# Kernel tuning notes

Hardware: AMD Instinct MI355X
Metric: run time of the kernel (lower is better)

The kernel has to match this reference:

```python
import jax, jax.numpy as jnp
import numpy as np

EMBED_DIM = 1024
NUM_HEADS = 16
HEAD_DIM = EMBED_DIM // NUM_HEADS
BATCH = 4
SEQ = 2048


def setup_inputs() -> dict:
    key = jax.random.key(0)
    k1, k2, k3 = jax.random.split(key, 3)
    scale = 0.02
    x = jax.random.normal(k1, (BATCH, SEQ, EMBED_DIM), dtype=jnp.float32)
    Wqkv = jax.random.normal(k2, (EMBED_DIM, 3 * EMBED_DIM), dtype=jnp.float32) * scale
    bqkv = jnp.zeros((3 * EMBED_DIM,), dtype=jnp.float32)
    Wout = jax.random.normal(k3, (EMBED_DIM, EMBED_DIM), dtype=jnp.float32) * scale
    bout = jnp.zeros((EMBED_DIM,), dtype=jnp.float32)
    # causal mask: 1 where attention is allowed (lower triangle), 0 elsewhere
    mask = jnp.tril(jnp.ones((SEQ, SEQ), dtype=jnp.int32))
    return {"x": x, "mask": mask, "Wqkv": Wqkv, "bqkv": bqkv, "Wout": Wout, "bout": bout}


def reference(x, mask, Wqkv, bqkv, Wout, bout):
    B, S, E = x.shape
    H, D = NUM_HEADS, HEAD_DIM
    qkv = x @ Wqkv + bqkv                      # [B,S,3E]
    qkv = qkv.reshape(B, S, 3, H, D)
    qkv = jnp.transpose(qkv, (2, 0, 3, 1, 4))  # [3,B,H,S,D]
    Q, K, V = qkv[0], qkv[1], qkv[2]
    scores = jnp.einsum('bhqd,bhkd->bhqk', Q, K) / jnp.sqrt(jnp.float32(D))
    scores = jnp.where(mask[None, None] == 0, jnp.float32(-jnp.inf), scores)
    attn = jax.nn.softmax(scores, axis=-1)     # dropout omitted (eval mode)
    out = jnp.einsum('bhqk,bhkd->bhqd', attn, V)
    out = jnp.transpose(out, (0, 2, 1, 3)).reshape(B, S, E)
    return out @ Wout + bout
```

## Files before the change

kernel.cpp:

```cpp
#include <hip/hip_runtime.h>

#define S_LEN 2048
#define NH    16
#define HD    64
#define EMB   1024
#define NB    4
#define MROWS (NB * S_LEN)

typedef __attribute__((ext_vector_type(8))) short  short8;
typedef __attribute__((ext_vector_type(4))) float  float4_t;
typedef __attribute__((ext_vector_type(4))) int    int4_t;
union U8 { int4_t i; short8 s; };

__device__ __forceinline__ unsigned short f2bf(float f) {
    unsigned int x = __float_as_uint(f);
    unsigned int r = (x + 0x7fffu + ((x >> 16) & 1u)) >> 16;
    return (unsigned short)r;
}

typedef const __attribute__((address_space(1))) unsigned int* gas_ptr;
typedef __attribute__((address_space(3))) unsigned int*       las_ptr;
__device__ __forceinline__ void gld_lds16(const void* g, void* l) {
    __builtin_amdgcn_global_load_lds((gas_ptr)g, (las_ptr)l, 16, 0, 0);
}

#define QSCALE 0.18033688011112042f

__global__ void cvt_f32_bf16(const float* __restrict__ in,
                             unsigned short* __restrict__ out, int n2) {
    int i = blockIdx.x * blockDim.x + threadIdx.x;
    if (i < n2) {
        float2 v = ((const float2*)in)[i];
        ushort2 o; o.x = f2bf(v.x); o.y = f2bf(v.y);
        ((ushort2*)out)[i] = o;
    }
}

__global__ void transpose_f32_bf16(const float* __restrict__ in,
                                   unsigned short* __restrict__ out, int R, int C) {
    __shared__ float tile[32][33];
    int n0 = blockIdx.x * 32, r0 = blockIdx.y * 32;
    int tx = threadIdx.x, ty = threadIdx.y;
#pragma unroll
    for (int i = 0; i < 4; ++i)
        tile[ty + i * 8][tx] = in[(size_t)(r0 + ty + i * 8) * C + n0 + tx];
    __syncthreads();
#pragma unroll
    for (int i = 0; i < 4; ++i)
        out[(size_t)(n0 + ty + i * 8) * R + r0 + tx] = f2bf(tile[tx][ty + i * 8]);
}

__global__ __launch_bounds__(256) void gemm_qkv(
    const unsigned short* __restrict__ X,
    const unsigned short* __restrict__ WT,
    const float* __restrict__ bias,
    unsigned short* __restrict__ Qb,
    unsigned short* __restrict__ Kb,
    unsigned short* __restrict__ VTb)
{
    __shared__ alignas(16) unsigned short As[128 * 32];
    __shared__ alignas(16) unsigned short Bs[128 * 32];
    const int K = 1024;
    int t = threadIdx.x;
    int wave = t >> 6, lane = t & 63, quad = lane >> 4, l = lane & 15;
    int bm = blockIdx.x * 128, bn = blockIdx.y * 128;
    int wm = (wave >> 1) * 64, wn = (wave & 1) * 64;

    float4_t z = {0.f, 0.f, 0.f, 0.f};
    float4_t acc[4][4];
#pragma unroll
    for (int i = 0; i < 4; ++i)
#pragma unroll
        for (int j = 0; j < 4; ++j) acc[i][j] = z;

    for (int kt = 0; kt < K / 32; ++kt) {
        int k0 = kt * 32;
        if (kt) __syncthreads();
#pragma unroll
        for (int it = 0; it < 2; ++it) {
            int c = t + 256 * it;
            int row = c >> 2, col = (c & 3) * 8;
            gld_lds16(&X [(size_t)(bm + row) * K + k0 + col], &As[c * 8]);
            gld_lds16(&WT[(size_t)(bn + row) * K + k0 + col], &Bs[c * 8]);
        }
        __syncthreads();
        short8 af[4], bfr[4];
#pragma unroll
        for (int i = 0; i < 4; ++i)
            af[i] = *(const short8*)&As[(wm + i * 16 + l) * 32 + quad * 8];
#pragma unroll
        for (int j = 0; j < 4; ++j)
            bfr[j] = *(const short8*)&Bs[(wn + j * 16 + l) * 32 + quad * 8];
#pragma unroll
        for (int i = 0; i < 4; ++i)
#pragma unroll
            for (int j = 0; j < 4; ++j)
                acc[i][j] = __builtin_amdgcn_mfma_f32_16x16x32_bf16(
                    af[i], bfr[j], acc[i][j], 0, 0, 0);
    }
#pragma unroll
    for (int j = 0; j < 4; ++j) {
        int gc = bn + wn + j * 16 + l;
        float bv = bias[gc];
        int which = gc >> 10, rem = gc & 1023;
        int h = rem >> 6, d = rem & 63;
        if (which == 2) {
            int bb = bm >> 11;
            size_t rowbase = ((size_t)(bb * NH + h) * HD + d) * S_LEN;
#pragma unroll
            for (int i = 0; i < 4; ++i) {
                unsigned int u0 = __float_as_uint(acc[i][j][0] + bv) + 0x8000u;
                unsigned int u1 = __float_as_uint(acc[i][j][1] + bv) + 0x8000u;
                unsigned int u2 = __float_as_uint(acc[i][j][2] + bv) + 0x8000u;
                unsigned int u3 = __float_as_uint(acc[i][j][3] + bv) + 0x8000u;
                uint2 vv;
                vv.x = __builtin_amdgcn_perm(u1, u0, 0x07060302u);
                vv.y = __builtin_amdgcn_perm(u3, u2, 0x07060302u);
                int s0 = (bm + wm + i * 16 + quad * 4) & 2047;
                int k6 = s0 & 63;
                int s0p = (s0 & ~63) | (((k6 >> 2) & 3) << 4) | (((k6 >> 4) & 3) << 2);
                *(uint2*)&VTb[rowbase + s0p] = vv;
            }
        } else {
#pragma unroll
            for (int i = 0; i < 4; ++i)
#pragma unroll
                for (int r = 0; r < 4; ++r) {
                    int gr = bm + wm + i * 16 + quad * 4 + r;
                    int b = gr >> 11, s = gr & 2047;
                    float ov = acc[i][j][r] + bv;
                    size_t bh2 = (size_t)(b * NH + h);
                    if (which == 0) Qb[(bh2 * S_LEN + s) * HD + d] = f2bf(ov * QSCALE);
                    else            Kb[(bh2 * S_LEN + s) * HD + d] = f2bf(ov);
                }
        }
    }
}

__global__ __launch_bounds__(256, 2) void flash_attn(
    const unsigned short* __restrict__ Qb,
    const unsigned short* __restrict__ Kb,
    const unsigned short* __restrict__ VTb,
    unsigned short* __restrict__ AO)
{
    __shared__ alignas(16) unsigned short smem[16384];

    int t = threadIdx.x, wave = t >> 6, lane = t & 63, quad = lane >> 4, cl = lane & 15;
    int blk = blockIdx.x;
    int bh = (blk & 7) + 8 * ((blk >> 3) & 7);
    int g = blk >> 6;
    int b = bh >> 4, h = bh & 15;
    int ci = (wave & 2) ? (62 - 2 * g + (wave & 1)) : (2 * g + (wave & 1));
    int qb = 32 * ci;
    int nkt = (ci >> 1) + 1;
    int nkt_max = 32 - g;

    const unsigned short* Qbase = Qb  + (size_t)bh * S_LEN * HD;
    const unsigned short* Kbase = Kb  + (size_t)bh * S_LEN * HD;
    const unsigned short* Vbase = VTb + (size_t)bh * HD * S_LEN;

    float4_t z = {0.f, 0.f, 0.f, 0.f};
    short8 onesf;
#pragma unroll
    for (int i = 0; i < 8; ++i) onesf[i] = (short)0x3F80;

    short8 bQ[2][2];
#pragma unroll
    for (int qt = 0; qt < 2; ++qt)
#pragma unroll
        for (int hh = 0; hh < 2; ++hh)
            bQ[qt][hh] = *(const short8*)&Qbase[(size_t)(qb + qt * 16 + cl) * HD + hh * 32 + quad * 8];

    float4_t acc[2][4], accs[2];
#pragma unroll
    for (int qt = 0; qt < 2; ++qt) {
        accs[qt] = z;
#pragma unroll
        for (int nb = 0; nb < 4; ++nb) acc[qt][nb] = z;
    }

    int koff0[4], koff1[4];
#pragma unroll
    for (int t4 = 0; t4 < 4; ++t4) {
        int row = t4 * 16 + cl, sw = row & 7;
        koff0[t4] = (row << 7) | ((quad ^ sw) << 4);
        koff1[t4] = (row << 7) | (((quad + 4) ^ sw) << 4);
    }
    int voffB[2][4];
#pragma unroll
    for (int p = 0; p < 2; ++p)
#pragma unroll
        for (int nb = 0; nb < 4; ++nb) {
            int row = nb * 16 + cl;
            voffB[p][nb] = 8192 + ((row << 7) | (((quad * 2 + p) ^ (row & 7)) << 4));
        }

    auto stage = [&](int u) {
        int key0 = u << 6;
        unsigned short* Kd = smem + (u & 1) * 8192;
        unsigned short* Vd = Kd + 4096;
#pragma unroll
        for (int i = 0; i < 2; ++i) {
            int s = t + 256 * i;
            int row = s >> 3, c16 = (s & 7) ^ (row & 7);
            gld_lds16(&Kbase[(size_t)(key0 + row) * HD + c16 * 8], &Kd[s * 8]);
            gld_lds16(&Vbase[(size_t)row * S_LEN + key0 + c16 * 8], &Vd[s * 8]);
        }
    };

    stage(0);
    for (int u = 0; u < nkt_max; ++u) {
        __syncthreads();
        if (u + 1 < nkt_max) stage(u + 1);
        if (u < nkt) {
            const char* Kc = (const char*)(smem + (u & 1) * 8192);
            int key0 = u << 6;
            short8 aK0[4], aK1[4];
#pragma unroll
            for (int t4 = 0; t4 < 4; ++t4) {
                aK0[t4] = *(const short8*)(Kc + koff0[t4]);
                aK1[t4] = *(const short8*)(Kc + koff1[t4]);
            }
            U8 bv[2][4];
#pragma unroll
            for (int p = 0; p < 2; ++p)
#pragma unroll
                for (int nb = 0; nb < 4; ++nb)
                    bv[p][nb].i = *(const int4_t*)(Kc + voffB[p][nb]);

            bool diag = (u == nkt - 1);
#pragma unroll
            for (int qt = 0; qt < 2; ++qt) {
                unsigned int pk[4][2];
#pragma unroll
                for (int t4 = 0; t4 < 4; ++t4) {
                    float4_t st = __builtin_amdgcn_mfma_f32_16x16x32_bf16(
                        aK1[t4], bQ[qt][1],
                        __builtin_amdgcn_mfma_f32_16x16x32_bf16(aK0[t4], bQ[qt][0], z, 0, 0, 0),
                        0, 0, 0);
                    unsigned int u4[4];
#pragma unroll
                    for (int r = 0; r < 4; ++r) {
                        float e = __builtin_amdgcn_exp2f(st[r]);
                        if (diag) {
                            int key = key0 + t4 * 16 + quad * 4 + r;
                            e = (key <= qb + qt * 16 + cl) ? e : 0.f;
                        }
                        u4[r] = __float_as_uint(e) + 0x8000u;
                    }
                    pk[t4][0] = __builtin_amdgcn_perm(u4[1], u4[0], 0x07060302u);
                    pk[t4][1] = __builtin_amdgcn_perm(u4[3], u4[2], 0x07060302u);
                }
#pragma unroll
                for (int p = 0; p < 2; ++p) {
                    U8 a; a.i = (int4_t){(int)pk[2 * p][0], (int)pk[2 * p][1],
                                         (int)pk[2 * p + 1][0], (int)pk[2 * p + 1][1]};
                    accs[qt] = __builtin_amdgcn_mfma_f32_16x16x32_bf16(
                        a.s, onesf, accs[qt], 0, 0, 0);
#pragma unroll
                    for (int nb = 0; nb < 4; ++nb)
                        acc[qt][nb] = __builtin_amdgcn_mfma_f32_16x16x32_bf16(
                            a.s, bv[p][nb].s, acc[qt][nb], 0, 0, 0);
                }
            }
        }
    }

    __syncthreads();
    unsigned short* stgw = smem + wave * 1088;

#pragma unroll
    for (int qt = 0; qt < 2; ++qt) {
        float fr[4];
#pragma unroll
        for (int r = 0; r < 4; ++r) fr[r] = 1.f / accs[qt][r];
#pragma unroll
        for (int nb = 0; nb < 4; ++nb)
#pragma unroll
            for (int r = 0; r < 4; ++r) {
                unsigned int uu = __float_as_uint(acc[qt][nb][r] * fr[r]) + 0x8000u;
                stgw[(quad * 4 + r) * 68 + nb * 16 + cl] = (unsigned short)(uu >> 16);
            }
#pragma unroll
        for (int pass = 0; pass < 4; ++pass) {
            int idx = pass * 64 + lane;
            int row = idx >> 4, part = idx & 15;
            ushort4 v = *(const ushort4*)&stgw[row * 68 + part * 4];
            *(ushort4*)&AO[((size_t)b * S_LEN + qb + qt * 16 + row) * EMB + h * HD + part * 4] = v;
        }
    }
}

__global__ __launch_bounds__(256) void gemm_out(
    const unsigned short* __restrict__ A,
    const unsigned short* __restrict__ WT,
    const float* __restrict__ bias,
    float* __restrict__ out)
{
    __shared__ alignas(16) unsigned short As[128 * 32];
    __shared__ alignas(16) unsigned short Bs[128 * 32];
    const int K = 1024;
    int t = threadIdx.x;
    int wave = t >> 6, lane = t & 63, quad = lane >> 4, l = lane & 15;
    int bm = blockIdx.x * 128, bn = blockIdx.y * 128;
    int wm = (wave >> 1) * 64, wn = (wave & 1) * 64;

    float4_t z = {0.f, 0.f, 0.f, 0.f};
    float4_t acc[4][4];
#pragma unroll
    for (int i = 0; i < 4; ++i)
#pragma unroll
        for (int j = 0; j < 4; ++j) acc[i][j] = z;

    for (int kt = 0; kt < K / 32; ++kt) {
        int k0 = kt * 32;
        if (kt) __syncthreads();
#pragma unroll
        for (int it = 0; it < 2; ++it) {
            int c = t + 256 * it;
            int row = c >> 2, col = (c & 3) * 8;
            gld_lds16(&A [(size_t)(bm + row) * K + k0 + col], &As[c * 8]);
            gld_lds16(&WT[(size_t)(bn + row) * K + k0 + col], &Bs[c * 8]);
        }
        __syncthreads();
        short8 af[4], bfr[4];
#pragma unroll
        for (int i = 0; i < 4; ++i)
            af[i] = *(const short8*)&As[(wm + i * 16 + l) * 32 + quad * 8];
#pragma unroll
        for (int j = 0; j < 4; ++j)
            bfr[j] = *(const short8*)&Bs[(wn + j * 16 + l) * 32 + quad * 8];
#pragma unroll
        for (int i = 0; i < 4; ++i)
#pragma unroll
            for (int j = 0; j < 4; ++j)
                acc[i][j] = __builtin_amdgcn_mfma_f32_16x16x32_bf16(
                    af[i], bfr[j], acc[i][j], 0, 0, 0);
    }
#pragma unroll
    for (int j = 0; j < 4; ++j) {
        int gc = bn + wn + j * 16 + l;
        float bv = bias[gc];
#pragma unroll
        for (int i = 0; i < 4; ++i) {
#pragma unroll
            for (int r = 0; r < 4; ++r) {
                int gr = bm + wm + i * 16 + quad * 4 + r;
                out[(size_t)gr * EMB + gc] = acc[i][j][r] + bv;
            }
        }
    }
}

extern "C" void kernel_launch(void* const* d_in, const int* in_sizes, int n_in,
                              void* d_out, int out_size, void* d_ws, size_t ws_size,
                              hipStream_t stream) {
    const float* x    = (const float*)d_in[0];
    const float* Wqkv = (const float*)d_in[2];
    const float* bqkv = (const float*)d_in[3];
    const float* Wout = (const float*)d_in[4];
    const float* bout = (const float*)d_in[5];
    float* out = (float*)d_out;

    char* ws = (char*)d_ws;
    const size_t SZ = (size_t)NB * NH * S_LEN * HD * 2;
    unsigned short* Qb    = (unsigned short*)(ws);
    unsigned short* Kb    = (unsigned short*)(ws + SZ);
    unsigned short* VTb   = (unsigned short*)(ws + 2 * SZ);
    unsigned short* Xb    = (unsigned short*)(ws + 3 * SZ);
    unsigned short* AO    = (unsigned short*)(ws + 3 * SZ);
    unsigned short* WqkvT = (unsigned short*)(ws + 4 * SZ);
    unsigned short* WoutT = (unsigned short*)(ws + 4 * SZ + (size_t)3 * EMB * EMB * 2);

    int n2 = MROWS * EMB / 2;
    cvt_f32_bf16<<<dim3((n2 + 255) / 256), 256, 0, stream>>>(x, Xb, n2);
    dim3 tb(32, 8);
    transpose_f32_bf16<<<dim3(3 * EMB / 32, EMB / 32), tb, 0, stream>>>(Wqkv, WqkvT, EMB, 3 * EMB);
    transpose_f32_bf16<<<dim3(EMB / 32, EMB / 32), tb, 0, stream>>>(Wout, WoutT, EMB, EMB);
    gemm_qkv<<<dim3(MROWS / 128, 3 * EMB / 128), 256, 0, stream>>>(Xb, WqkvT, bqkv, Qb, Kb, VTb);
    flash_attn<<<dim3(1024), 256, 0, stream>>>(Qb, Kb, VTb, AO);
    gemm_out<<<dim3(MROWS / 128, EMB / 128), 256, 0, stream>>>(AO, WoutT, bout, out);
}
```

Baseline: 270.0 us.

## Triple-buffer K/V tiles with explicit vmcnt waits and templated diagonal path

Moves the flash-attention K/V staging from double to triple buffering in LDS. Tiles are prefetched two steps ahead, and the loop waits with explicit s_waitcnt vmcnt plus a raw s_barrier instead of __syncthreads, so global-to-LDS loads overlap more compute. The diagonal masking is split into a compile-time template so non-diagonal tiles skip the mask code, and the P conversion to bf16 now uses the v_cvt_pk_bf16_f32 instruction. LDS use grows from 32KB to 48KB per block, which may limit occupancy, and the hand-written vmcnt counts must match the number of outstanding loads.

```diff
diff --git a/kernel.cpp b/kernel.cpp
--- a/kernel.cpp
+++ b/kernel.cpp
@@ -18,11 +18,19 @@
     return (unsigned short)r;
 }
 
+__device__ __forceinline__ unsigned int cvtpk_bf16(float lo, float hi) {
+    unsigned int r;
+    asm("v_cvt_pk_bf16_f32 %0, %1, %2" : "=v"(r) : "v"(lo), "v"(hi));
+    return r;
+}
+
 typedef const __attribute__((address_space(1))) unsigned int* gas_ptr;
 typedef __attribute__((address_space(3))) unsigned int*       las_ptr;
 __device__ __forceinline__ void gld_lds16(const void* g, void* l) {
     __builtin_amdgcn_global_load_lds((gas_ptr)g, (las_ptr)l, 16, 0, 0);
 }
+
+template<bool B> struct BoolC { static constexpr bool v = B; };
 
 #define QSCALE 0.18033688011112042f
 
@@ -143,7 +151,7 @@
     const unsigned short* __restrict__ VTb,
     unsigned short* __restrict__ AO)
 {
-    __shared__ alignas(16) unsigned short smem[16384];
+    __shared__ alignas(16) unsigned short smem[24576];
 
     int t = threadIdx.x, wave = t >> 6, lane = t & 63, quad = lane >> 4, cl = lane & 15;
     int blk = blockIdx.x;
@@ -195,9 +203,9 @@
             voffB[p][nb] = 8192 + ((row << 7) | (((quad * 2 + p) ^ (row & 7)) << 4));
         }
 
-    auto stage = [&](int u) {
-        int key0 = u << 6;
-        unsigned short* Kd = smem + (u & 1) * 8192;
+    auto stage = [&](int kt, int slot) {
+        int key0 = kt << 6;
+        unsigned short* Kd = smem + slot * 8192;
         unsigned short* Vd = Kd + 4096;
 #pragma unroll
         for (int i = 0; i < 2; ++i) {
@@ -208,62 +216,75 @@
         }
     };
 
-    stage(0);
+    auto compute = [&](auto DIAGC, int slot, int key0) {
+        constexpr bool DIAG = decltype(DIAGC)::v;
+        const char* Kc = (const char*)(smem + slot * 8192);
+        short8 aK0[4], aK1[4];
+#pragma unroll
+        for (int t4 = 0; t4 < 4; ++t4) {
+            aK0[t4] = *(const short8*)(Kc + koff0[t4]);
+            aK1[t4] = *(const short8*)(Kc + koff1[t4]);
+        }
+        U8 bv[2][4];
+#pragma unroll
+        for (int p = 0; p < 2; ++p)
+#pragma unroll
+            for (int nb = 0; nb < 4; ++nb)
+                bv[p][nb].i = *(const int4_t*)(Kc + voffB[p][nb]);
+
+#pragma unroll
+        for (int qt = 0; qt < 2; ++qt) {
+            unsigned int pk[4][2];
+#pragma unroll
+            for (int t4 = 0; t4 < 4; ++t4) {
+                float4_t st = __builtin_amdgcn_mfma_f32_16x16x32_bf16(
+                    aK1[t4], bQ[qt][1],
+                    __builtin_amdgcn_mfma_f32_16x16x32_bf16(aK0[t4], bQ[qt][0], z, 0, 0, 0),
+                    0, 0, 0);
+                float e[4];
+#pragma unroll
+                for (int r = 0; r < 4; ++r) {
+                    e[r] = __builtin_amdgcn_exp2f(st[r]);
+                    if (DIAG) {
+                        int key = key0 + t4 * 16 + quad * 4 + r;
+                        e[r] = (key <= qb + qt * 16 + cl) ? e[r] : 0.f;
+                    }
+                }
+                pk[t4][0] = cvtpk_bf16(e[0], e[1]);
+                pk[t4][1] = cvtpk_bf16(e[2], e[3]);
+            }
+#pragma unroll
+            for (int p = 0; p < 2; ++p) {
+                U8 a; a.i = (int4_t){(int)pk[2 * p][0], (int)pk[2 * p][1],
+                                     (int)pk[2 * p + 1][0], (int)pk[2 * p + 1][1]};
+                accs[qt] = __builtin_amdgcn_mfma_f32_16x16x32_bf16(
+                    a.s, onesf, accs[qt], 0, 0, 0);
+#pragma unroll
+                for (int nb = 0; nb < 4; ++nb)
+                    acc[qt][nb] = __builtin_amdgcn_mfma_f32_16x16x32_bf16(
+                        a.s, bv[p][nb].s, acc[qt][nb], 0, 0, 0);
+            }
+        }
+    };
+
+    stage(0, 0);
+    if (nkt_max > 1) stage(1, 1);
+    int cb = 0, sb = 2;
     for (int u = 0; u < nkt_max; ++u) {
-        __syncthreads();
-        if (u + 1 < nkt_max) stage(u + 1);
+        if (u + 1 < nkt_max) {
+            asm volatile("s_waitcnt vmcnt(4)" ::: "memory");
+        } else {
+            asm volatile("s_waitcnt vmcnt(0)" ::: "memory");
+        }
+        __builtin_amdgcn_s_barrier();
+        __builtin_amdgcn_sched_barrier(0);
+        if (u + 2 < nkt_max) stage(u + 2, sb);
         if (u < nkt) {
-            const char* Kc = (const char*)(smem + (u & 1) * 8192);
-            int key0 = u << 6;
-            short8 aK0[4], aK1[4];
-#pragma unroll
-            for (int t4 = 0; t4 < 4; ++t4) {
-                aK0[t4] = *(const short8*)(Kc + koff0[t4]);
-                aK1[t4] = *(const short8*)(Kc + koff1[t4]);
-            }
-            U8 bv[2][4];
-#pragma unroll
-            for (int p = 0; p < 2; ++p)
-#pragma unroll
-                for (int nb = 0; nb < 4; ++nb)
-                    bv[p][nb].i = *(const int4_t*)(Kc + voffB[p][nb]);
-
-            bool diag = (u == nkt - 1);
-#pragma unroll
-            for (int qt = 0; qt < 2; ++qt) {
-                unsigned int pk[4][2];
-#pragma unroll
-                for (int t4 = 0; t4 < 4; ++t4) {
-                    float4_t st = __builtin_amdgcn_mfma_f32_16x16x32_bf16(
-                        aK1[t4], bQ[qt][1],
-                        __builtin_amdgcn_mfma_f32_16x16x32_bf16(aK0[t4], bQ[qt][0], z, 0, 0, 0),
-                        0, 0, 0);
-                    unsigned int u4[4];
-#pragma unroll
-                    for (int r = 0; r < 4; ++r) {
-                        float e = __builtin_amdgcn_exp2f(st[r]);
-                        if (diag) {
-                            int key = key0 + t4 * 16 + quad * 4 + r;
-                            e = (key <= qb + qt * 16 + cl) ? e : 0.f;
-                        }
-                        u4[r] = __float_as_uint(e) + 0x8000u;
-                    }
-                    pk[t4][0] = __builtin_amdgcn_perm(u4[1], u4[0], 0x07060302u);
-                    pk[t4][1] = __builtin_amdgcn_perm(u4[3], u4[2], 0x07060302u);
-                }
-#pragma unroll
-                for (int p = 0; p < 2; ++p) {
-                    U8 a; a.i = (int4_t){(int)pk[2 * p][0], (int)pk[2 * p][1],
-                                         (int)pk[2 * p + 1][0], (int)pk[2 * p + 1][1]};
-                    accs[qt] = __builtin_amdgcn_mfma_f32_16x16x32_bf16(
-                        a.s, onesf, accs[qt], 0, 0, 0);
-#pragma unroll
-                    for (int nb = 0; nb < 4; ++nb)
-                        acc[qt][nb] = __builtin_amdgcn_mfma_f32_16x16x32_bf16(
-                            a.s, bv[p][nb].s, acc[qt][nb], 0, 0, 0);
-                }
-            }
-        }
+            if (u == nkt - 1) compute(BoolC<true>{},  cb, u << 6);
+            else              compute(BoolC<false>{}, cb, u << 6);
+        }
+        cb = (cb == 2) ? 0 : cb + 1;
+        sb = (sb == 2) ? 0 : sb + 1;
     }
 
     __syncthreads();
```

Result: faster. 248.4 us (-8.0%).
